# Kernel optimization log

Measured on AMD Instinct MI355X. Metric: run time of the kernel, lower is better.

Reference implementation:

```python
import jax, jax.numpy as jnp
import numpy as np
import math

B, S, D, H = 8, 512, 768, 12
DK = D // H
NEG = 1.0e9


def _split_heads(x):
    # [B,S,D] -> [B,H,S,DK]
    b, s, d = x.shape
    return x.reshape(b, s, H, DK).transpose(0, 2, 1, 3)


def setup_inputs() -> dict:
    key = jax.random.key(0)
    ks = jax.random.split(key, 16)
    std = 1.0 / math.sqrt(D)
    query = jax.random.normal(ks[0], (B, S, D), jnp.float32)
    key_t = jax.random.normal(ks[1], (B, S, D), jnp.float32)
    # mask: 0 for valid tokens, -10000 sentinel for padding
    mask = jnp.where(jax.random.bernoulli(ks[2], 0.9, (B, S)), 0.0, -10000.0).astype(jnp.float32)
    # span targets: binary [H,B,S,S]
    span_matrix = jax.random.bernoulli(ks[3], 0.1, (H, B, S, S)).astype(jnp.float32)
    def lin(i):
        W = jax.random.normal(ks[4 + 2 * i], (D, D), jnp.float32) * std
        b = jax.random.normal(ks[5 + 2 * i], (D,), jnp.float32) * std
        return W, b
    Wql, bql = lin(0)
    Wkl, bkl = lin(1)
    Wqr, bqr = lin(2)
    Wkr, bkr = lin(3)
    Wq, bq = lin(4)
    Wk, bk = lin(5)
    return dict(query=query, key=key_t, mask=mask, span_matrix=span_matrix,
                Wql=Wql, bql=bql, Wkl=Wkl, bkl=bkl,
                Wqr=Wqr, bqr=bqr, Wkr=Wkr, bkr=bkr,
                Wq=Wq, bq=bq, Wk=Wk, bk=bk)


def _forward(query, key, mask, span_matrix,
             Wql, bql, Wkl, bkl, Wqr, bqr, Wkr, bkr, Wq, bq, Wk, bk):
    scale = 1.0 / math.sqrt(D)  # note: original scales by sqrt(model_dim), not sqrt(d_k)
    idx = jnp.arange(S)
    lower = idx[None, :] <= idx[:, None]  # [S,S] lower-triangular incl. diag
    left_boundary = jnp.where(lower, 0.0, NEG)   # 1e9 above diagonal
    right_boundary = left_boundary.T             # 1e9 below diagonal

    # left branch
    ql = _split_heads(query @ Wql + bql) * scale
    kl = _split_heads(key @ Wkl + bkl)
    left_scores = jnp.einsum('bhqd,bhkd->bhqk', ql, kl)
    theta_l = jax.nn.softmax(left_scores - left_boundary, axis=-1)

    # right branch
    qr = _split_heads(query @ Wqr + bqr) * scale
    kr = _split_heads(key @ Wkr + bkr)
    right_scores = jnp.einsum('bhqd,bhkd->bhqk', qr, kr)
    theta_r = jax.nn.softmax(right_scores - right_boundary, axis=-1)

    # theta_l @ upperTri == inclusive cumsum over last axis (O(S) instead of O(S^2) matmul)
    soft_Mask_l = jnp.cumsum(theta_l, axis=-1)
    # theta_r @ lowerTri == inclusive reverse cumsum over last axis
    soft_Mask_r = jnp.cumsum(theta_r[..., ::-1], axis=-1)[..., ::-1]
    soft_Mask = soft_Mask_l * soft_Mask_r

    # main attention
    q = _split_heads(query @ Wq + bq) * scale
    k = _split_heads(key @ Wk + bk)
    att_scores = jnp.einsum('bhqd,bhkd->bhqk', q, k)
    row_mask = jnp.where(mask == -10000.0, NEG, mask)  # [B,S]
    att_scores = att_scores - row_mask[:, None, :, None] - row_mask[:, None, None, :]
    p_local_attn = jax.nn.softmax(att_scores * soft_Mask, axis=-1)

    # per-head BCE between sigmoid(attn) and span targets; mean over heads of per-head means
    # == global mean since every head has the same element count
    span = span_matrix.transpose(1, 0, 2, 3)  # [B,H,S,S]
    p_sig = jax.nn.sigmoid(p_local_attn)      # in (0.5, 0.732], logs are safe
    bce = -(span * jnp.log(p_sig) + (1.0 - span) * jnp.log1p(-p_sig))
    span_loss = jnp.mean(bce)
    return p_local_attn, span_loss


def reference(query, key, mask, span_matrix,
              Wql, bql, Wkl, bkl, Wqr, bqr, Wkr, bkr, Wq, bq, Wk, bk):
    return _forward(query, key, mask, span_matrix,
                    Wql, bql, Wkl, bkl, Wqr, bqr, Wkr, bkr, Wq, bq, Wk, bk)
```

## Files before the change

### kernel.cpp

```cpp
#include <hip/hip_runtime.h>
#include <math.h>

#define BB 8
#define SS 512
#define DD 768
#define HH 12
#define DKK 64
#define NTOK (BB*SS)
#define NELEM (25165824ull)
#define NPROJ 3145728
#define WSZ   589824
#define SCALEQ 0.03608439182435161f

typedef unsigned short u16;
typedef short short8 __attribute__((ext_vector_type(8)));
typedef float f32x4 __attribute__((ext_vector_type(4)));
typedef unsigned short u16x4 __attribute__((ext_vector_type(4)));

#define MFMA16 __builtin_amdgcn_mfma_f32_16x16x32_bf16

__device__ inline u16 f32_to_bf16(float f) {
    unsigned int u = __float_as_uint(f);
    unsigned int r = u + 0x7fffu + ((u >> 16) & 1u);
    return (u16)(r >> 16);
}
__device__ inline float bf16_to_f32(u16 h) {
    return __uint_as_float(((unsigned int)h) << 16);
}

__device__ __forceinline__ void gld16(const u16* g, u16* l) {
    __builtin_amdgcn_global_load_lds(
        (const __attribute__((address_space(1))) unsigned int*)g,
        (__attribute__((address_space(3))) unsigned int*)l, 16, 0, 0);
}

__global__ __launch_bounds__(256)
void cast_wT(const float* __restrict__ W0, const float* __restrict__ W1,
             const float* __restrict__ W2, const float* __restrict__ W3,
             const float* __restrict__ W4, const float* __restrict__ W5,
             u16* __restrict__ WTh, u16* __restrict__ WTl,
             float* __restrict__ lossp)
{
    __shared__ float tile[32][33];
    if (blockIdx.x == 0 && blockIdx.y == 0 && blockIdx.z == 0 && threadIdx.x == 0)
        *lossp = 0.0f;
    const int z = blockIdx.z;
    const float* W;
    switch (z) {
        case 0: W = W0; break; case 1: W = W1; break; case 2: W = W2; break;
        case 3: W = W3; break; case 4: W = W4; break; default: W = W5; break;
    }
    u16* th = WTh + (size_t)z * WSZ;
    u16* tl = WTl + (size_t)z * WSZ;
    const int t = threadIdx.x;
    const int k0 = blockIdx.y * 32, n0 = blockIdx.x * 32;
    const int rr = t >> 3, c0 = (t & 7) * 4;

    float4 v = *(const float4*)(W + (size_t)(k0 + rr) * DD + n0 + c0);
    tile[rr][c0 + 0] = v.x; tile[rr][c0 + 1] = v.y;
    tile[rr][c0 + 2] = v.z; tile[rr][c0 + 3] = v.w;
    __syncthreads();

    u16x4 hw, lw;
#pragma unroll
    for (int i = 0; i < 4; ++i) {
        float f = tile[c0 + i][rr];
        u16 hi = f32_to_bf16(f);
        hw[i] = hi;
        lw[i] = f32_to_bf16(f - bf16_to_f32(hi));
    }
    size_t o = (size_t)(n0 + rr) * DD + k0 + c0;
    *(u16x4*)&th[o] = hw;
    *(u16x4*)&tl[o] = lw;
}

__global__ __launch_bounds__(256)
void cast_X(const float* __restrict__ query, const float* __restrict__ key,
            u16* __restrict__ Xh, u16* __restrict__ Xl)
{
    const float* src = blockIdx.y ? key : query;
    u16* dh = Xh + (size_t)blockIdx.y * NPROJ;
    u16* dl = Xl + (size_t)blockIdx.y * NPROJ;
    size_t i0 = ((size_t)blockIdx.x * 256 + threadIdx.x) * 8;
    float f[8];
    *(float4*)&f[0] = *(const float4*)(src + i0);
    *(float4*)&f[4] = *(const float4*)(src + i0 + 4);
    short8 h, l;
#pragma unroll
    for (int i = 0; i < 8; ++i) {
        u16 hi = f32_to_bf16(f[i]);
        h[i] = (short)hi;
        l[i] = (short)f32_to_bf16(f[i] - bf16_to_f32(hi));
    }
    *(short8*)&dh[i0] = h;
    *(short8*)&dl[i0] = l;
}

__global__ __launch_bounds__(256)
void proj_gemm_gld(const u16* __restrict__ Xh, const u16* __restrict__ Xl,
                   const u16* __restrict__ WTh, const u16* __restrict__ WTl,
                   const float* __restrict__ b0, const float* __restrict__ b1,
                   const float* __restrict__ b2, const float* __restrict__ b3,
                   const float* __restrict__ b4, const float* __restrict__ b5,
                   u16* __restrict__ Ph, u16* __restrict__ Pl)
{
    __shared__ alignas(16) u16 Ash[128][32];
    __shared__ alignas(16) u16 Asl[128][32];
    __shared__ alignas(16) u16 Bsh[128][32];
    __shared__ alignas(16) u16 Bsl[128][32];

    const int z = blockIdx.z;
    const float* bias;
    switch (z) {
        case 0: bias = b0; break; case 1: bias = b1; break; case 2: bias = b2; break;
        case 3: bias = b3; break; case 4: bias = b4; break; default: bias = b5; break;
    }
    const float scl = (z & 1) ? 1.0f : SCALEQ;
    const u16* Ah_g = Xh + (size_t)(z & 1) * NPROJ;
    const u16* Al_g = Xl + (size_t)(z & 1) * NPROJ;
    const u16* WThz = WTh + (size_t)z * WSZ;
    const u16* WTlz = WTl + (size_t)z * WSZ;
    u16* Ch = Ph + (size_t)z * NPROJ;
    u16* Cl = Pl + (size_t)z * NPROJ;
    const bool wlo = (z < 4);

    const int t = threadIdx.x;
    const int w = t >> 6, l = t & 63, quad = l >> 4, ln = l & 15;
    const int m0 = blockIdx.y * 128, n0 = blockIdx.x * 128;
    const int wm = (w & 1) * 64, wn = (w >> 1) * 64;

    const int srow = w * 16 + (l >> 2);
    const int scol = (l & 3) * 8;
    const u16* gAh = Ah_g + (size_t)(m0 + srow) * DD + scol;
    const u16* gAl = Al_g + (size_t)(m0 + srow) * DD + scol;
    const u16* gBh = WThz + (size_t)(n0 + srow) * DD + scol;
    const u16* gBl = WTlz + (size_t)(n0 + srow) * DD + scol;
    u16* lAh0 = &Ash[w * 16][0];      u16* lAh1 = &Ash[w * 16 + 64][0];
    u16* lAl0 = &Asl[w * 16][0];      u16* lAl1 = &Asl[w * 16 + 64][0];
    u16* lBh0 = &Bsh[w * 16][0];      u16* lBh1 = &Bsh[w * 16 + 64][0];
    u16* lBl0 = &Bsl[w * 16][0];      u16* lBl1 = &Bsl[w * 16 + 64][0];
    const size_t rstep = (size_t)64 * DD;

    f32x4 acc[4][4];
#pragma unroll
    for (int i = 0; i < 4; ++i)
#pragma unroll
        for (int jj = 0; jj < 4; ++jj) acc[i][jj] = (f32x4){0.f, 0.f, 0.f, 0.f};

    for (int k0 = 0; k0 < DD; k0 += 32) {
        gld16(gAh + k0, lAh0);  gld16(gAh + k0 + rstep, lAh1);
        gld16(gBh + k0, lBh0);  gld16(gBh + k0 + rstep, lBh1);
        if (wlo) {
            gld16(gAl + k0, lAl0);  gld16(gAl + k0 + rstep, lAl1);
            gld16(gBl + k0, lBl0);  gld16(gBl + k0 + rstep, lBl1);
        }
        __syncthreads();

        short8 afh[4], afl[4], bfh[4], bfl[4];
#pragma unroll
        for (int mt = 0; mt < 4; ++mt)
            afh[mt] = *(const short8*)&Ash[wm + mt * 16 + ln][quad * 8];
#pragma unroll
        for (int nt = 0; nt < 4; ++nt)
            bfh[nt] = *(const short8*)&Bsh[wn + nt * 16 + ln][quad * 8];
        if (wlo) {
#pragma unroll
            for (int mt = 0; mt < 4; ++mt)
                afl[mt] = *(const short8*)&Asl[wm + mt * 16 + ln][quad * 8];
#pragma unroll
            for (int nt = 0; nt < 4; ++nt)
                bfl[nt] = *(const short8*)&Bsl[wn + nt * 16 + ln][quad * 8];
        }
#pragma unroll
        for (int mt = 0; mt < 4; ++mt)
#pragma unroll
            for (int nt = 0; nt < 4; ++nt) {
                acc[mt][nt] = MFMA16(bfh[nt], afh[mt], acc[mt][nt], 0, 0, 0);
                if (wlo) {
                    acc[mt][nt] = MFMA16(bfl[nt], afh[mt], acc[mt][nt], 0, 0, 0);
                    acc[mt][nt] = MFMA16(bfh[nt], afl[mt], acc[mt][nt], 0, 0, 0);
                }
            }
        __syncthreads();
    }

#pragma unroll
    for (int nt = 0; nt < 4; ++nt) {
        const int nb4 = n0 + wn + nt * 16 + quad * 4;
        float4 bias4 = *(const float4*)(bias + nb4);
        float bv[4] = {bias4.x, bias4.y, bias4.z, bias4.w};
#pragma unroll
        for (int mt = 0; mt < 4; ++mt) {
            const int m = m0 + wm + mt * 16 + ln;
            u16x4 hv, lv;
#pragma unroll
            for (int reg = 0; reg < 4; ++reg) {
                float c = (acc[mt][nt][reg] + bv[reg]) * scl;
                u16 hi = f32_to_bf16(c);
                hv[reg] = hi;
                lv[reg] = f32_to_bf16(c - bf16_to_f32(hi));
            }
            size_t o = (size_t)m * DD + nb4;
            *(u16x4*)&Ch[o] = hv;
            if (wlo) *(u16x4*)&Cl[o] = lv;
        }
    }
}

__global__ __launch_bounds__(256)
void proj_gemm_mfma(const float* __restrict__ query, const float* __restrict__ key,
                    const u16* __restrict__ WTh, const u16* __restrict__ WTl,
                    const float* __restrict__ b0, const float* __restrict__ b1,
                    const float* __restrict__ b2, const float* __restrict__ b3,
                    const float* __restrict__ b4, const float* __restrict__ b5,
                    u16* __restrict__ Ph, u16* __restrict__ Pl)
{
    __shared__ alignas(16) u16 Ash[128][40];
    __shared__ alignas(16) u16 Asl[128][40];
    __shared__ alignas(16) u16 Bsh[128][40];
    __shared__ alignas(16) u16 Bsl[128][40];

    const int z = blockIdx.z;
    const float* X = (z & 1) ? key : query;
    const float* bias;
    switch (z) {
        case 0: bias = b0; break; case 1: bias = b1; break; case 2: bias = b2; break;
        case 3: bias = b3; break; case 4: bias = b4; break; default: bias = b5; break;
    }
    const float scl = (z & 1) ? 1.0f : SCALEQ;
    const u16* WThz = WTh + (size_t)z * WSZ;
    const u16* WTlz = WTl + (size_t)z * WSZ;
    u16* Ch = Ph + (size_t)z * NPROJ;
    u16* Cl = Pl + (size_t)z * NPROJ;
    const bool wlo = (z < 4);

    const int t = threadIdx.x;
    const int w = t >> 6, l = t & 63, quad = l >> 4, ln = l & 15;
    const int m0 = blockIdx.y * 128, n0 = blockIdx.x * 128;
    const int wm = (w & 1) * 64, wn = (w >> 1) * 64;

    const int arow = t >> 1, akoff = (t & 1) * 16;
    const int brow = t >> 1, bkoff = (t & 1) * 16;

    f32x4 acc[4][4];
#pragma unroll
    for (int i = 0; i < 4; ++i)
#pragma unroll
        for (int jj = 0; jj < 4; ++jj) acc[i][jj] = (f32x4){0.f, 0.f, 0.f, 0.f};

    for (int k0 = 0; k0 < DD; k0 += 32) {
        {
            const float* asrc = X + (size_t)(m0 + arow) * DD + k0 + akoff;
            float fa[16];
            *(float4*)&fa[0]  = *(const float4*)(asrc + 0);
            *(float4*)&fa[4]  = *(const float4*)(asrc + 4);
            *(float4*)&fa[8]  = *(const float4*)(asrc + 8);
            *(float4*)&fa[12] = *(const float4*)(asrc + 12);
            short8 h0, h1, l0, l1;
#pragma unroll
            for (int i = 0; i < 8; ++i) {
                u16 hi = f32_to_bf16(fa[i]);
                h0[i] = (short)hi;
                l0[i] = (short)f32_to_bf16(fa[i] - bf16_to_f32(hi));
                u16 hi2 = f32_to_bf16(fa[8 + i]);
                h1[i] = (short)hi2;
                l1[i] = (short)f32_to_bf16(fa[8 + i] - bf16_to_f32(hi2));
            }
            *(short8*)&Ash[arow][akoff]     = h0;
            *(short8*)&Ash[arow][akoff + 8] = h1;
            *(short8*)&Asl[arow][akoff]     = l0;
            *(short8*)&Asl[arow][akoff + 8] = l1;
        }
        {
            const u16* bhp = WThz + (size_t)(n0 + brow) * DD + k0 + bkoff;
            const u16* blp = WTlz + (size_t)(n0 + brow) * DD + k0 + bkoff;
            *(uint4*)&Bsh[brow][bkoff]     = *(const uint4*)(bhp);
            *(uint4*)&Bsh[brow][bkoff + 8] = *(const uint4*)(bhp + 8);
            *(uint4*)&Bsl[brow][bkoff]     = *(const uint4*)(blp);
            *(uint4*)&Bsl[brow][bkoff + 8] = *(const uint4*)(blp + 8);
        }
        __syncthreads();

        short8 afh[4], afl[4], bfh[4], bfl[4];
#pragma unroll
        for (int mt = 0; mt < 4; ++mt) {
            afh[mt] = *(const short8*)&Ash[wm + mt * 16 + ln][quad * 8];
            afl[mt] = *(const short8*)&Asl[wm + mt * 16 + ln][quad * 8];
        }
#pragma unroll
        for (int nt = 0; nt < 4; ++nt) {
            bfh[nt] = *(const short8*)&Bsh[wn + nt * 16 + ln][quad * 8];
            bfl[nt] = *(const short8*)&Bsl[wn + nt * 16 + ln][quad * 8];
        }
#pragma unroll
        for (int mt = 0; mt < 4; ++mt)
#pragma unroll
            for (int nt = 0; nt < 4; ++nt) {
                acc[mt][nt] = MFMA16(bfh[nt], afh[mt], acc[mt][nt], 0, 0, 0);
                acc[mt][nt] = MFMA16(bfl[nt], afh[mt], acc[mt][nt], 0, 0, 0);
                acc[mt][nt] = MFMA16(bfh[nt], afl[mt], acc[mt][nt], 0, 0, 0);
            }
        __syncthreads();
    }

#pragma unroll
    for (int nt = 0; nt < 4; ++nt) {
        const int nb4 = n0 + wn + nt * 16 + quad * 4;
        float4 bias4 = *(const float4*)(bias + nb4);
        float bv[4] = {bias4.x, bias4.y, bias4.z, bias4.w};
#pragma unroll
        for (int mt = 0; mt < 4; ++mt) {
            const int m = m0 + wm + mt * 16 + ln;
            u16x4 hv, lv;
#pragma unroll
            for (int reg = 0; reg < 4; ++reg) {
                float c = (acc[mt][nt][reg] + bv[reg]) * scl;
                u16 hi = f32_to_bf16(c);
                hv[reg] = hi;
                lv[reg] = f32_to_bf16(c - bf16_to_f32(hi));
            }
            size_t o = (size_t)m * DD + nb4;
            *(u16x4*)&Ch[o] = hv;
            if (wlo) *(u16x4*)&Cl[o] = lv;
        }
    }
}

#define CPITCH 532
__global__ __launch_bounds__(512, 4)
void attn_mfma(const u16* __restrict__ Ph, const u16* __restrict__ Pl,
               const float* __restrict__ mask, const float* __restrict__ span,
               float* __restrict__ outp, float* __restrict__ lossp)
{
    __shared__ float curb[16][CPITCH];
    __shared__ float lred[8];

    const int t = threadIdx.x;
    const int blk = blockIdx.x;
    const int qt = blk & 31;
    const int bh = blk >> 5;
    const int b = bh / HH, h = bh % HH;
    const int w = t >> 6, l = t & 63, quad = l >> 4, ln = l & 15;
    const int r = t >> 5, j = t & 31;
    const int qrow = qt * 16 + r;
    const int bb = 33 * (j >> 1) + 16 * (j & 1);
    const int cB = j * 16;

    float smbr[16];

    auto compute_scores = [&](const u16* Qh, const u16* Ql,
                              const u16* Kh, const u16* Kl, bool use_lo) {
        const size_t qoff = (size_t)(b * SS + qt * 16 + ln) * DD + h * DKK + quad * 8;
        short8 ah0 = *(const short8*)(Qh + qoff);
        short8 ah1 = *(const short8*)(Qh + qoff + 32);
        short8 al0 = ah0, al1 = ah1;
        if (use_lo) {
            al0 = *(const short8*)(Ql + qoff);
            al1 = *(const short8*)(Ql + qoff + 32);
        }
        const size_t koff = (size_t)(b * SS + w * 16 + ln) * DD + h * DKK + quad * 8;
        const u16* kb = Kh + koff;
        const u16* klb = use_lo ? (Kl + koff) : kb;
        __syncthreads();
#pragma unroll
        for (int kc = 0; kc < 4; ++kc) {
            const size_t off = (size_t)kc * (128 * DD);
            short8 bh0 = *(const short8*)(kb + off);
            short8 bh1 = *(const short8*)(kb + off + 32);
            f32x4 acc = (f32x4){0.f, 0.f, 0.f, 0.f};
            acc = MFMA16(ah0, bh0, acc, 0, 0, 0);
            acc = MFMA16(ah1, bh1, acc, 0, 0, 0);
            if (use_lo) {
                short8 bl0 = *(const short8*)(klb + off);
                short8 bl1 = *(const short8*)(klb + off + 32);
                acc = MFMA16(ah0, bl0, acc, 0, 0, 0);
                acc = MFMA16(ah1, bl1, acc, 0, 0, 0);
                acc = MFMA16(al0, bh0, acc, 0, 0, 0);
                acc = MFMA16(al1, bh1, acc, 0, 0, 0);
            }
            const int cb = kc * 128 + w * 16 + ln;
            const int ci = cb + (cb >> 5);
#pragma unroll
            for (int reg = 0; reg < 4; ++reg)
                curb[quad * 4 + reg][ci] = acc[reg];
        }
        __syncthreads();
    };

    compute_scores(Ph + 0 * (size_t)NPROJ, Pl + 0 * (size_t)NPROJ,
                   Ph + 1 * (size_t)NPROJ, Pl + 1 * (size_t)NPROJ, true);
    {
        float e[16];
        float mx = -3.0e38f;
#pragma unroll
        for (int u = 0; u < 16; ++u) {
            float v = curb[r][bb + u];
            e[u] = v;
            if (cB + u <= qrow && v > mx) mx = v;
        }
#pragma unroll
        for (int off = 16; off >= 1; off >>= 1) mx = fmaxf(mx, __shfl_xor(mx, off));
        float s = 0.0f;
#pragma unroll
        for (int u = 0; u < 16; ++u) {
            float ev = (cB + u <= qrow) ? __expf(e[u] - mx) : 0.0f;
            s += ev;
            e[u] = s;
        }
        float incl = s;
#pragma unroll
        for (int off = 1; off < 32; off <<= 1) {
            float ww = __shfl_up(incl, off, 32);
            if (j >= off) incl += ww;
        }
        float offset = incl - s;
        float inv = 1.0f / __shfl(incl, 31, 32);
#pragma unroll
        for (int u = 0; u < 16; ++u) smbr[u] = (offset + e[u]) * inv;
    }

    compute_scores(Ph + 2 * (size_t)NPROJ, Pl + 2 * (size_t)NPROJ,
                   Ph + 3 * (size_t)NPROJ, Pl + 3 * (size_t)NPROJ, true);
    {
        float e[16];
        float mx = -3.0e38f;
#pragma unroll
        for (int u = 0; u < 16; ++u) {
            float v = curb[r][bb + u];
            e[u] = v;
            if (cB + u >= qrow && v > mx) mx = v;
        }
#pragma unroll
        for (int off = 16; off >= 1; off >>= 1) mx = fmaxf(mx, __shfl_xor(mx, off));
        float s = 0.0f;
#pragma unroll
        for (int u = 15; u >= 0; --u) {
            float ev = (cB + u >= qrow) ? __expf(e[u] - mx) : 0.0f;
            s += ev;
            e[u] = s;
        }
        float incl = s;
#pragma unroll
        for (int off = 1; off < 32; off <<= 1) {
            float ww = __shfl_down(incl, off, 32);
            if (j + off < 32) incl += ww;
        }
        float offset = incl - s;
        float inv = 1.0f / __shfl(incl, 0, 32);
#pragma unroll
        for (int u = 0; u < 16; ++u) smbr[u] *= (offset + e[u]) * inv;

#pragma unroll
        for (int u = 0; u < 16; ++u) curb[r][bb + u] = smbr[u];
        __syncthreads();
#pragma unroll
        for (int u = 0; u < 16; ++u) smbr[u] = curb[r][u * 33 + j];
    }

    compute_scores(Ph + 4 * (size_t)NPROJ, (const u16*)0,
                   Ph + 5 * (size_t)NPROJ, (const u16*)0, false);
    {
        float mv  = mask[b * SS + qrow];
        float rmq = (mv == -10000.0f) ? 1.0e9f : mv;
        float vb[16];
        float mx = -3.0e38f;
#pragma unroll
        for (int u = 0; u < 16; ++u) {
            int c = u * 32 + j;
            float mk  = mask[b * SS + c];
            float rmk = (mk == -10000.0f) ? 1.0e9f : mk;
            float v = (curb[r][u * 33 + j] - rmq - rmk) * smbr[u];
            vb[u] = v;
            mx = fmaxf(mx, v);
        }
#pragma unroll
        for (int off = 16; off >= 1; off >>= 1) mx = fmaxf(mx, __shfl_xor(mx, off));
        float sum = 0.0f;
#pragma unroll
        for (int u = 0; u < 16; ++u) {
            float ev = __expf(vb[u] - mx);
            vb[u] = ev; sum += ev;
        }
#pragma unroll
        for (int off = 16; off >= 1; off >>= 1) sum += __shfl_xor(sum, off);
        float inv = 1.0f / sum;

        float* orow = outp + (((size_t)(b * HH + h) * SS + qrow)) * SS;
        const float* sprow = span + (((size_t)(h * BB + b) * SS + qrow)) * SS;
        float lsum = 0.0f;
#pragma unroll
        for (int u = 0; u < 16; ++u) {
            int c = u * 32 + j;
            float p = vb[u] * inv;
            orow[c] = p;
            float s = sprow[c];
            lsum += __logf(1.0f + __expf(-p)) + (1.0f - s) * p;
        }
#pragma unroll
        for (int off = 32; off >= 1; off >>= 1) lsum += __shfl_xor(lsum, off);
        if ((t & 63) == 0) lred[t >> 6] = lsum;
        __syncthreads();
        if (t == 0) {
            float tot = 0.0f;
#pragma unroll
            for (int i = 0; i < 8; ++i) tot += lred[i];
            atomicAdd(lossp, tot * (float)(1.0 / 25165824.0));
        }
    }
}

extern "C" void kernel_launch(void* const* d_in, const int* in_sizes, int n_in,
                              void* d_out, int out_size, void* d_ws, size_t ws_size,
                              hipStream_t stream)
{
    const float* query = (const float*)d_in[0];
    const float* key_t = (const float*)d_in[1];
    const float* mask  = (const float*)d_in[2];
    const float* span  = (const float*)d_in[3];
    const float* Wql = (const float*)d_in[4];  const float* bql = (const float*)d_in[5];
    const float* Wkl = (const float*)d_in[6];  const float* bkl = (const float*)d_in[7];
    const float* Wqr = (const float*)d_in[8];  const float* bqr = (const float*)d_in[9];
    const float* Wkr = (const float*)d_in[10]; const float* bkr = (const float*)d_in[11];
    const float* Wq  = (const float*)d_in[12]; const float* bq  = (const float*)d_in[13];
    const float* Wk  = (const float*)d_in[14]; const float* bk  = (const float*)d_in[15];

    float* out = (float*)d_out;
    float* lossp = out + NELEM;

    u16* ws16 = (u16*)d_ws;
    u16* WTh = ws16;
    u16* WTl = WTh + (size_t)6 * WSZ;
    u16* Ph  = WTl + (size_t)6 * WSZ;
    u16* Pl  = Ph + (size_t)6 * NPROJ;
    u16* Xh  = Pl + (size_t)4 * NPROJ;
    u16* Xl  = Xh + (size_t)2 * NPROJ;
    const size_t need_big = ((size_t)12 * WSZ + (size_t)14 * NPROJ) * 2;
    const bool bigws = ws_size >= need_big;

    cast_wT<<<dim3(24, 24, 6), dim3(256), 0, stream>>>(
        Wql, Wkl, Wqr, Wkr, Wq, Wk, WTh, WTl, lossp);

    if (bigws) {
        cast_X<<<dim3(1536, 2), dim3(256), 0, stream>>>(query, key_t, Xh, Xl);
        proj_gemm_gld<<<dim3(DD / 128, NTOK / 128, 6), dim3(256), 0, stream>>>(
            Xh, Xl, WTh, WTl, bql, bkl, bqr, bkr, bq, bk, Ph, Pl);
    } else {
        proj_gemm_mfma<<<dim3(DD / 128, NTOK / 128, 6), dim3(256), 0, stream>>>(
            query, key_t, WTh, WTl, bql, bkl, bqr, bkr, bq, bk, Ph, Pl);
    }

    attn_mfma<<<dim3(96 * 32), dim3(512), 0, stream>>>(
        Ph, Pl, mask, span, out, lossp);
}
```

Baseline: 471.6 us.

## Use 1024-thread attention blocks with one wavefront per query row

The attention kernel moves from 512 to 1024 threads per block. Each of the 16 wavefronts now computes 32 key columns with two MFMA tiles instead of four and owns one full query row. Row reductions and prefix scans therefore use full 64-lane wavefront shuffles instead of 32-lane half-wave segments. The aim is more parallelism and fewer per-thread elements and registers per row, at the cost of larger blocks, longer shuffle chains and possibly lower occupancy per CU.

```diff
diff --git a/kernel.cpp b/kernel.cpp
--- a/kernel.cpp
+++ b/kernel.cpp
@@ -327,13 +327,13 @@
 }
 
 #define CPITCH 532
-__global__ __launch_bounds__(512, 4)
+__global__ __launch_bounds__(1024, 8)
 void attn_mfma(const u16* __restrict__ Ph, const u16* __restrict__ Pl,
                const float* __restrict__ mask, const float* __restrict__ span,
                float* __restrict__ outp, float* __restrict__ lossp)
 {
     __shared__ float curb[16][CPITCH];
-    __shared__ float lred[8];
+    __shared__ float lred[16];
 
     const int t = threadIdx.x;
     const int blk = blockIdx.x;
@@ -341,12 +341,11 @@
     const int bh = blk >> 5;
     const int b = bh / HH, h = bh % HH;
     const int w = t >> 6, l = t & 63, quad = l >> 4, ln = l & 15;
-    const int r = t >> 5, j = t & 31;
-    const int qrow = qt * 16 + r;
-    const int bb = 33 * (j >> 1) + 16 * (j & 1);
-    const int cB = j * 16;
-
-    float smbr[16];
+    const int qrow = qt * 16 + w;
+    const int c0 = l * 8;
+    const int swb = c0 + (l >> 2);
+
+    float smbr[8];
 
     auto compute_scores = [&](const u16* Qh, const u16* Ql,
                               const u16* Kh, const u16* Kl, bool use_lo) {
@@ -358,27 +357,25 @@
             al0 = *(const short8*)(Ql + qoff);
             al1 = *(const short8*)(Ql + qoff + 32);
         }
-        const size_t koff = (size_t)(b * SS + w * 16 + ln) * DD + h * DKK + quad * 8;
-        const u16* kb = Kh + koff;
-        const u16* klb = use_lo ? (Kl + koff) : kb;
-        __syncthreads();
-#pragma unroll
-        for (int kc = 0; kc < 4; ++kc) {
-            const size_t off = (size_t)kc * (128 * DD);
-            short8 bh0 = *(const short8*)(kb + off);
-            short8 bh1 = *(const short8*)(kb + off + 32);
+        const size_t koff = (size_t)(b * SS + w * 32 + ln) * DD + h * DKK + quad * 8;
+        __syncthreads();
+#pragma unroll
+        for (int nt = 0; nt < 2; ++nt) {
+            const size_t off = koff + (size_t)(nt * 16) * DD;
+            short8 bh0 = *(const short8*)(Kh + off);
+            short8 bh1 = *(const short8*)(Kh + off + 32);
             f32x4 acc = (f32x4){0.f, 0.f, 0.f, 0.f};
             acc = MFMA16(ah0, bh0, acc, 0, 0, 0);
             acc = MFMA16(ah1, bh1, acc, 0, 0, 0);
             if (use_lo) {
-                short8 bl0 = *(const short8*)(klb + off);
-                short8 bl1 = *(const short8*)(klb + off + 32);
+                short8 bl0 = *(const short8*)(Kl + off);
+                short8 bl1 = *(const short8*)(Kl + off + 32);
                 acc = MFMA16(ah0, bl0, acc, 0, 0, 0);
                 acc = MFMA16(ah1, bl1, acc, 0, 0, 0);
                 acc = MFMA16(al0, bh0, acc, 0, 0, 0);
                 acc = MFMA16(al1, bh1, acc, 0, 0, 0);
             }
-            const int cb = kc * 128 + w * 16 + ln;
+            const int cb = w * 32 + nt * 16 + ln;
             const int ci = cb + (cb >> 5);
 #pragma unroll
             for (int reg = 0; reg < 4; ++reg)
@@ -390,71 +387,74 @@
     compute_scores(Ph + 0 * (size_t)NPROJ, Pl + 0 * (size_t)NPROJ,
                    Ph + 1 * (size_t)NPROJ, Pl + 1 * (size_t)NPROJ, true);
     {
-        float e[16];
+        float e[8];
         float mx = -3.0e38f;
 #pragma unroll
-        for (int u = 0; u < 16; ++u) {
-            float v = curb[r][bb + u];
+        for (int u = 0; u < 8; ++u) {
+            float v = curb[w][swb + u];
             e[u] = v;
-            if (cB + u <= qrow && v > mx) mx = v;
-        }
-#pragma unroll
-        for (int off = 16; off >= 1; off >>= 1) mx = fmaxf(mx, __shfl_xor(mx, off));
+            if (c0 + u <= qrow && v > mx) mx = v;
+        }
+#pragma unroll
+        for (int off = 32; off >= 1; off >>= 1) mx = fmaxf(mx, __shfl_xor(mx, off));
         float s = 0.0f;
 #pragma unroll
-        for (int u = 0; u < 16; ++u) {
-            float ev = (cB + u <= qrow) ? __expf(e[u] - mx) : 0.0f;
+        for (int u = 0; u < 8; ++u) {
+            float ev = (c0 + u <= qrow) ? __expf(e[u] - mx) : 0.0f;
             s += ev;
             e[u] = s;
         }
         float incl = s;
 #pragma unroll
-        for (int off = 1; off < 32; off <<= 1) {
-            float ww = __shfl_up(incl, off, 32);
-            if (j >= off) incl += ww;
+        for (int off = 1; off < 64; off <<= 1) {
+            float ww = __shfl_up(incl, off, 64);
+            if (l >= off) incl += ww;
         }
         float offset = incl - s;
-        float inv = 1.0f / __shfl(incl, 31, 32);
-#pragma unroll
-        for (int u = 0; u < 16; ++u) smbr[u] = (offset + e[u]) * inv;
+        float inv = 1.0f / __shfl(incl, 63, 64);
+#pragma unroll
+        for (int u = 0; u < 8; ++u) smbr[u] = (offset + e[u]) * inv;
     }
 
     compute_scores(Ph + 2 * (size_t)NPROJ, Pl + 2 * (size_t)NPROJ,
                    Ph + 3 * (size_t)NPROJ, Pl + 3 * (size_t)NPROJ, true);
     {
-        float e[16];
+        float e[8];
         float mx = -3.0e38f;
 #pragma unroll
-        for (int u = 0; u < 16; ++u) {
-            float v = curb[r][bb + u];
+        for (int u = 0; u < 8; ++u) {
+            float v = curb[w][swb + u];
             e[u] = v;
-            if (cB + u >= qrow && v > mx) mx = v;
-        }
-#pragma unroll
-        for (int off = 16; off >= 1; off >>= 1) mx = fmaxf(mx, __shfl_xor(mx, off));
+            if (c0 + u >= qrow && v > mx) mx = v;
+        }
+#pragma unroll
+        for (int off = 32; off >= 1; off >>= 1) mx = fmaxf(mx, __shfl_xor(mx, off));
         float s = 0.0f;
 #pragma unroll
-        for (int u = 15; u >= 0; --u) {
-            float ev = (cB + u >= qrow) ? __expf(e[u] - mx) : 0.0f;
+        for (int u = 7; u >= 0; --u) {
+            float ev = (c0 + u >= qrow) ? __expf(e[u] - mx) : 0.0f;
             s += ev;
             e[u] = s;
         }
         float incl = s;
 #pragma unroll
-        for (int off = 1; off < 32; off <<= 1) {
-            float ww = __shfl_down(incl, off, 32);
-            if (j + off < 32) incl += ww;
+        for (int off = 1; off < 64; off <<= 1) {
+            float ww = __shfl_down(incl, off, 64);
+            if (l + off < 64) incl += ww;
         }
         float offset = incl - s;
-        float inv = 1.0f / __shfl(incl, 0, 32);
-#pragma unroll
-        for (int u = 0; u < 16; ++u) smbr[u] *= (offset + e[u]) * inv;
-
-#pragma unroll
-        for (int u = 0; u < 16; ++u) curb[r][bb + u] = smbr[u];
-        __syncthreads();
-#pragma unroll
-        for (int u = 0; u < 16; ++u) smbr[u] = curb[r][u * 33 + j];
+        float inv = 1.0f / __shfl(incl, 0, 64);
+#pragma unroll
+        for (int u = 0; u < 8; ++u) smbr[u] *= (offset + e[u]) * inv;
+
+#pragma unroll
+        for (int u = 0; u < 8; ++u) curb[w][swb + u] = smbr[u];
+        __syncthreads();
+#pragma unroll
+        for (int u = 0; u < 8; ++u) {
+            int c = u * 64 + l;
+            smbr[u] = curb[w][c + (c >> 5)];
+        }
     }
 
     compute_scores(Ph + 4 * (size_t)NPROJ, (const u16*)0,
@@ -462,35 +462,35 @@
     {
         float mv  = mask[b * SS + qrow];
         float rmq = (mv == -10000.0f) ? 1.0e9f : mv;
-        float vb[16];
+        float vb[8];
         float mx = -3.0e38f;
 #pragma unroll
-        for (int u = 0; u < 16; ++u) {
-            int c = u * 32 + j;
+        for (int u = 0; u < 8; ++u) {
+            int c = u * 64 + l;
             float mk  = mask[b * SS + c];
             float rmk = (mk == -10000.0f) ? 1.0e9f : mk;
-            float v = (curb[r][u * 33 + j] - rmq - rmk) * smbr[u];
+            float v = (curb[w][c + (c >> 5)] - rmq - rmk) * smbr[u];
             vb[u] = v;
             mx = fmaxf(mx, v);
         }
 #pragma unroll
-        for (int off = 16; off >= 1; off >>= 1) mx = fmaxf(mx, __shfl_xor(mx, off));
+        for (int off = 32; off >= 1; off >>= 1) mx = fmaxf(mx, __shfl_xor(mx, off));
         float sum = 0.0f;
 #pragma unroll
-        for (int u = 0; u < 16; ++u) {
+        for (int u = 0; u < 8; ++u) {
             float ev = __expf(vb[u] - mx);
             vb[u] = ev; sum += ev;
         }
 #pragma unroll
-        for (int off = 16; off >= 1; off >>= 1) sum += __shfl_xor(sum, off);
+        for (int off = 32; off >= 1; off >>= 1) sum += __shfl_xor(sum, off);
         float inv = 1.0f / sum;
 
         float* orow = outp + (((size_t)(b * HH + h) * SS + qrow)) * SS;
         const float* sprow = span + (((size_t)(h * BB + b) * SS + qrow)) * SS;
         float lsum = 0.0f;
 #pragma unroll
-        for (int u = 0; u < 16; ++u) {
-            int c = u * 32 + j;
+        for (int u = 0; u < 8; ++u) {
+            int c = u * 64 + l;
             float p = vb[u] * inv;
             orow[c] = p;
             float s = sprow[c];
@@ -498,12 +498,12 @@
         }
 #pragma unroll
         for (int off = 32; off >= 1; off >>= 1) lsum += __shfl_xor(lsum, off);
-        if ((t & 63) == 0) lred[t >> 6] = lsum;
+        if (l == 0) lred[w] = lsum;
         __syncthreads();
         if (t == 0) {
             float tot = 0.0f;
 #pragma unroll
-            for (int i = 0; i < 8; ++i) tot += lred[i];
+            for (int i = 0; i < 16; ++i) tot += lred[i];
             atomicAdd(lossp, tot * (float)(1.0 / 25165824.0));
         }
     }
@@ -549,6 +549,6 @@
             query, key_t, WTh, WTl, bql, bkl, bqr, bkr, bq, bk, Ph, Pl);
     }
 
-    attn_mfma<<<dim3(96 * 32), dim3(512), 0, stream>>>(
+    attn_mfma<<<dim3(96 * 32), dim3(1024), 0, stream>>>(
         Ph, Pl, mask, span, out, lossp);
 }
```

New measurement: 493.6 us. 4.7% more time.

## Interleave left/right score MFMAs, prefetch main K, move BCE loss to separate kernel

Applied to the files above, without the earlier changes.

The attention kernel now computes the left and right branch score tiles together into two shared buffers and preloads the main-branch Q and K fragments before the softmax/cumsum stages, removing syncs between the stages and overlapping loads with compute. The BCE loss is split out into its own kernel that re-reads the output probabilities and span targets with float4 loads. This costs double the shared memory per block, which may lower occupancy, and an extra pass that reads the full output tensor back from memory.

```diff
diff --git a/kernel.cpp b/kernel.cpp
--- a/kernel.cpp
+++ b/kernel.cpp
@@ -329,11 +329,10 @@
 #define CPITCH 532
 __global__ __launch_bounds__(512, 4)
 void attn_mfma(const u16* __restrict__ Ph, const u16* __restrict__ Pl,
-               const float* __restrict__ mask, const float* __restrict__ span,
-               float* __restrict__ outp, float* __restrict__ lossp)
+               const float* __restrict__ mask, float* __restrict__ outp)
 {
-    __shared__ float curb[16][CPITCH];
-    __shared__ float lred[8];
+    __shared__ float curbL[16][CPITCH];
+    __shared__ float curbR[16][CPITCH];
 
     const int t = threadIdx.x;
     const int blk = blockIdx.x;
@@ -348,53 +347,82 @@
 
     float smbr[16];
 
-    auto compute_scores = [&](const u16* Qh, const u16* Ql,
-                              const u16* Kh, const u16* Kl, bool use_lo) {
-        const size_t qoff = (size_t)(b * SS + qt * 16 + ln) * DD + h * DKK + quad * 8;
-        short8 ah0 = *(const short8*)(Qh + qoff);
-        short8 ah1 = *(const short8*)(Qh + qoff + 32);
-        short8 al0 = ah0, al1 = ah1;
-        if (use_lo) {
-            al0 = *(const short8*)(Ql + qoff);
-            al1 = *(const short8*)(Ql + qoff + 32);
-        }
-        const size_t koff = (size_t)(b * SS + w * 16 + ln) * DD + h * DKK + quad * 8;
-        const u16* kb = Kh + koff;
-        const u16* klb = use_lo ? (Kl + koff) : kb;
-        __syncthreads();
+    const size_t qoff = (size_t)(b * SS + qt * 16 + ln) * DD + h * DKK + quad * 8;
+    const size_t koff = (size_t)(b * SS + w * 16 + ln) * DD + h * DKK + quad * 8;
+
+    const u16* QhL = Ph + 0 * (size_t)NPROJ;  const u16* QlL = Pl + 0 * (size_t)NPROJ;
+    const u16* KhL = Ph + 1 * (size_t)NPROJ;  const u16* KlL = Pl + 1 * (size_t)NPROJ;
+    const u16* QhR = Ph + 2 * (size_t)NPROJ;  const u16* QlR = Pl + 2 * (size_t)NPROJ;
+    const u16* KhR = Ph + 3 * (size_t)NPROJ;  const u16* KlR = Pl + 3 * (size_t)NPROJ;
+    const u16* QhM = Ph + 4 * (size_t)NPROJ;
+    const u16* KhM = Ph + 5 * (size_t)NPROJ;
+
+    {
+        short8 aLh0 = *(const short8*)(QhL + qoff);
+        short8 aLh1 = *(const short8*)(QhL + qoff + 32);
+        short8 aLl0 = *(const short8*)(QlL + qoff);
+        short8 aLl1 = *(const short8*)(QlL + qoff + 32);
+        short8 aRh0 = *(const short8*)(QhR + qoff);
+        short8 aRh1 = *(const short8*)(QhR + qoff + 32);
+        short8 aRl0 = *(const short8*)(QlR + qoff);
+        short8 aRl1 = *(const short8*)(QlR + qoff + 32);
 #pragma unroll
         for (int kc = 0; kc < 4; ++kc) {
-            const size_t off = (size_t)kc * (128 * DD);
-            short8 bh0 = *(const short8*)(kb + off);
-            short8 bh1 = *(const short8*)(kb + off + 32);
-            f32x4 acc = (f32x4){0.f, 0.f, 0.f, 0.f};
-            acc = MFMA16(ah0, bh0, acc, 0, 0, 0);
-            acc = MFMA16(ah1, bh1, acc, 0, 0, 0);
-            if (use_lo) {
-                short8 bl0 = *(const short8*)(klb + off);
-                short8 bl1 = *(const short8*)(klb + off + 32);
-                acc = MFMA16(ah0, bl0, acc, 0, 0, 0);
-                acc = MFMA16(ah1, bl1, acc, 0, 0, 0);
-                acc = MFMA16(al0, bh0, acc, 0, 0, 0);
-                acc = MFMA16(al1, bh1, acc, 0, 0, 0);
-            }
+            const size_t off = koff + (size_t)kc * (128 * DD);
             const int cb = kc * 128 + w * 16 + ln;
             const int ci = cb + (cb >> 5);
-#pragma unroll
-            for (int reg = 0; reg < 4; ++reg)
-                curb[quad * 4 + reg][ci] = acc[reg];
-        }
-        __syncthreads();
-    };
-
-    compute_scores(Ph + 0 * (size_t)NPROJ, Pl + 0 * (size_t)NPROJ,
-                   Ph + 1 * (size_t)NPROJ, Pl + 1 * (size_t)NPROJ, true);
+            {
+                short8 bh0 = *(const short8*)(KhL + off);
+                short8 bh1 = *(const short8*)(KhL + off + 32);
+                short8 bl0 = *(const short8*)(KlL + off);
+                short8 bl1 = *(const short8*)(KlL + off + 32);
+                f32x4 acc = (f32x4){0.f, 0.f, 0.f, 0.f};
+                acc = MFMA16(aLh0, bh0, acc, 0, 0, 0);
+                acc = MFMA16(aLh1, bh1, acc, 0, 0, 0);
+                acc = MFMA16(aLh0, bl0, acc, 0, 0, 0);
+                acc = MFMA16(aLh1, bl1, acc, 0, 0, 0);
+                acc = MFMA16(aLl0, bh0, acc, 0, 0, 0);
+                acc = MFMA16(aLl1, bh1, acc, 0, 0, 0);
+#pragma unroll
+                for (int reg = 0; reg < 4; ++reg)
+                    curbL[quad * 4 + reg][ci] = acc[reg];
+            }
+            {
+                short8 bh0 = *(const short8*)(KhR + off);
+                short8 bh1 = *(const short8*)(KhR + off + 32);
+                short8 bl0 = *(const short8*)(KlR + off);
+                short8 bl1 = *(const short8*)(KlR + off + 32);
+                f32x4 acc = (f32x4){0.f, 0.f, 0.f, 0.f};
+                acc = MFMA16(aRh0, bh0, acc, 0, 0, 0);
+                acc = MFMA16(aRh1, bh1, acc, 0, 0, 0);
+                acc = MFMA16(aRh0, bl0, acc, 0, 0, 0);
+                acc = MFMA16(aRh1, bl1, acc, 0, 0, 0);
+                acc = MFMA16(aRl0, bh0, acc, 0, 0, 0);
+                acc = MFMA16(aRl1, bh1, acc, 0, 0, 0);
+#pragma unroll
+                for (int reg = 0; reg < 4; ++reg)
+                    curbR[quad * 4 + reg][ci] = acc[reg];
+            }
+        }
+    }
+    __syncthreads();
+
+    short8 aMh0 = *(const short8*)(QhM + qoff);
+    short8 aMh1 = *(const short8*)(QhM + qoff + 32);
+    short8 km0[4], km1[4];
+#pragma unroll
+    for (int kc = 0; kc < 4; ++kc) {
+        const size_t off = koff + (size_t)kc * (128 * DD);
+        km0[kc] = *(const short8*)(KhM + off);
+        km1[kc] = *(const short8*)(KhM + off + 32);
+    }
+
     {
         float e[16];
         float mx = -3.0e38f;
 #pragma unroll
         for (int u = 0; u < 16; ++u) {
-            float v = curb[r][bb + u];
+            float v = curbL[r][bb + u];
             e[u] = v;
             if (cB + u <= qrow && v > mx) mx = v;
         }
@@ -419,14 +447,12 @@
         for (int u = 0; u < 16; ++u) smbr[u] = (offset + e[u]) * inv;
     }
 
-    compute_scores(Ph + 2 * (size_t)NPROJ, Pl + 2 * (size_t)NPROJ,
-                   Ph + 3 * (size_t)NPROJ, Pl + 3 * (size_t)NPROJ, true);
     {
         float e[16];
         float mx = -3.0e38f;
 #pragma unroll
         for (int u = 0; u < 16; ++u) {
-            float v = curb[r][bb + u];
+            float v = curbR[r][bb + u];
             e[u] = v;
             if (cB + u >= qrow && v > mx) mx = v;
         }
@@ -451,14 +477,26 @@
         for (int u = 0; u < 16; ++u) smbr[u] *= (offset + e[u]) * inv;
 
 #pragma unroll
-        for (int u = 0; u < 16; ++u) curb[r][bb + u] = smbr[u];
-        __syncthreads();
-#pragma unroll
-        for (int u = 0; u < 16; ++u) smbr[u] = curb[r][u * 33 + j];
-    }
-
-    compute_scores(Ph + 4 * (size_t)NPROJ, (const u16*)0,
-                   Ph + 5 * (size_t)NPROJ, (const u16*)0, false);
+        for (int u = 0; u < 16; ++u) curbL[r][bb + u] = smbr[u];
+    }
+    __syncthreads();
+
+#pragma unroll
+    for (int u = 0; u < 16; ++u) smbr[u] = curbL[r][u * 33 + j];
+
+#pragma unroll
+    for (int kc = 0; kc < 4; ++kc) {
+        const int cb = kc * 128 + w * 16 + ln;
+        const int ci = cb + (cb >> 5);
+        f32x4 acc = (f32x4){0.f, 0.f, 0.f, 0.f};
+        acc = MFMA16(aMh0, km0[kc], acc, 0, 0, 0);
+        acc = MFMA16(aMh1, km1[kc], acc, 0, 0, 0);
+#pragma unroll
+        for (int reg = 0; reg < 4; ++reg)
+            curbR[quad * 4 + reg][ci] = acc[reg];
+    }
+    __syncthreads();
+
     {
         float mv  = mask[b * SS + qrow];
         float rmq = (mv == -10000.0f) ? 1.0e9f : mv;
@@ -469,7 +507,7 @@
             int c = u * 32 + j;
             float mk  = mask[b * SS + c];
             float rmk = (mk == -10000.0f) ? 1.0e9f : mk;
-            float v = (curb[r][u * 33 + j] - rmq - rmk) * smbr[u];
+            float v = (curbR[r][u * 33 + j] - rmq - rmk) * smbr[u];
             vb[u] = v;
             mx = fmaxf(mx, v);
         }
@@ -486,26 +524,42 @@
         float inv = 1.0f / sum;
 
         float* orow = outp + (((size_t)(b * HH + h) * SS + qrow)) * SS;
-        const float* sprow = span + (((size_t)(h * BB + b) * SS + qrow)) * SS;
-        float lsum = 0.0f;
-#pragma unroll
-        for (int u = 0; u < 16; ++u) {
-            int c = u * 32 + j;
-            float p = vb[u] * inv;
-            orow[c] = p;
-            float s = sprow[c];
-            lsum += __logf(1.0f + __expf(-p)) + (1.0f - s) * p;
-        }
-#pragma unroll
-        for (int off = 32; off >= 1; off >>= 1) lsum += __shfl_xor(lsum, off);
-        if ((t & 63) == 0) lred[t >> 6] = lsum;
-        __syncthreads();
-        if (t == 0) {
-            float tot = 0.0f;
-#pragma unroll
-            for (int i = 0; i < 8; ++i) tot += lred[i];
-            atomicAdd(lossp, tot * (float)(1.0 / 25165824.0));
-        }
+#pragma unroll
+        for (int u = 0; u < 16; ++u)
+            orow[u * 32 + j] = vb[u] * inv;
+    }
+}
+
+__global__ __launch_bounds__(256)
+void bce_loss(const float* __restrict__ outp, const float* __restrict__ span,
+              float* __restrict__ lossp)
+{
+    __shared__ float lred[4];
+    const int sp = blockIdx.y;
+    const int h = sp >> 3, b = sp & 7;
+    const size_t sbase = (size_t)sp * (SS * SS);
+    const size_t obase = (size_t)(b * HH + h) * (SS * SS);
+    const int t = threadIdx.x;
+
+    float lsum = 0.0f;
+#pragma unroll
+    for (int it = 0; it < 4; ++it) {
+        size_t v4 = ((size_t)it * 64 + blockIdx.x) * 256 + t;
+        float4 pv = *(const float4*)(outp + obase + v4 * 4);
+        float4 sv = *(const float4*)(span + sbase + v4 * 4);
+        float p0 = pv.x, p1 = pv.y, p2 = pv.z, p3 = pv.w;
+        lsum += __logf(1.0f + __expf(-p0)) + (1.0f - sv.x) * p0;
+        lsum += __logf(1.0f + __expf(-p1)) + (1.0f - sv.y) * p1;
+        lsum += __logf(1.0f + __expf(-p2)) + (1.0f - sv.z) * p2;
+        lsum += __logf(1.0f + __expf(-p3)) + (1.0f - sv.w) * p3;
+    }
+#pragma unroll
+    for (int off = 32; off >= 1; off >>= 1) lsum += __shfl_xor(lsum, off);
+    if ((t & 63) == 0) lred[t >> 6] = lsum;
+    __syncthreads();
+    if (t == 0) {
+        float tot = lred[0] + lred[1] + lred[2] + lred[3];
+        atomicAdd(lossp, tot * (float)(1.0 / 25165824.0));
     }
 }
 
@@ -550,5 +604,8 @@
     }
 
     attn_mfma<<<dim3(96 * 32), dim3(512), 0, stream>>>(
-        Ph, Pl, mask, span, out, lossp);
-}
+        Ph, Pl, mask, out);
+
+    bce_loss<<<dim3(64, 96), dim3(256), 0, stream>>>(
+        out, span, lossp);
+}
```

Result: slower. 525.1 us (+11.4%).
